# Optimization experiments

Hardware: AMD Instinct MI355X
Metric: run time of the kernel (lower is better)

Reference implementation:

```python
import jax, jax.numpy as jnp
import numpy as np

B, N, F_IN, F_OUT = 8, 4096, 256, 256


def setup_inputs() -> dict:
    key = jax.random.key(0)
    k1, k2, k3 = jax.random.split(key, 3)
    H = jax.random.normal(k1, (B, N, F_IN), dtype=jnp.float32)
    W = jax.random.normal(k2, (F_IN, F_OUT), dtype=jnp.float32) * (1.0 / np.sqrt(F_IN))
    A = jax.random.normal(k3, (N, N), dtype=jnp.float32) * (1.414 * np.sqrt(2.0 / (N + N)))
    return {"H": H, "W": W, "A": A}


def reference(H, W, A):
    # HW: [B, N, F_out]
    HW = jnp.einsum('bnf,fo->bno', H, W)
    # symmetrize + relu -> nonneg adjacency [N, N]
    A_norm = jax.nn.relu((A + A.T) * 0.5)
    # degree and inverse sqrt (inf -> 0 for isolated nodes)
    D = jnp.sum(A_norm, axis=1)
    D_safe = jnp.where(D > 0, D, 1.0)
    d_inv_sqrt = jnp.where(D > 0, D_safe ** -0.5, 0.0)
    # L_norm = I - D^{-1/2} A D^{-1/2}  (diagonal scaling, no dense diag matmul)
    DAD = d_inv_sqrt[:, None] * A_norm * d_inv_sqrt[None, :]
    L_norm = jnp.eye(N, dtype=H.dtype) - DAD
    # output = relu(L_norm @ HW): [B, N, F_out]
    out = jnp.einsum('nm,bmo->bno', L_norm, HW)
    return jax.nn.relu(out)
```

## Files before the change

kernel.cpp:

```cpp
#include <hip/hip_runtime.h>
#include <stdint.h>

#define N_NODES 4096
#define F_DIM   256
#define BATCH   8

typedef __attribute__((ext_vector_type(8))) __bf16 bf16x8;
typedef __attribute__((ext_vector_type(4))) float  f32x4;
typedef __attribute__((ext_vector_type(8))) unsigned short u16x8;

typedef const __attribute__((address_space(1))) void* gas1_t;
typedef __attribute__((address_space(3))) void*       las3_t;

__device__ __forceinline__ void stage16(const void* g, void* l) {
  __builtin_amdgcn_global_load_lds((gas1_t)g, (las3_t)l, 16, 0, 0);
}

__device__ __forceinline__ unsigned short f2bf(float f) {
  union { float f; uint32_t u; } v; v.f = f;
  uint32_t u = v.u;
  return (unsigned short)((u + 0x7FFFu + ((u >> 16) & 1u)) >> 16);
}
__device__ __forceinline__ float bf2f(unsigned short u) {
  union { uint32_t u; float f; } v; v.u = ((uint32_t)u) << 16;
  return v.f;
}

__global__ __launch_bounds__(256) void k_pre(const float* __restrict__ A,
                                             unsigned short* __restrict__ Sb,
                                             float* __restrict__ D,
                                             const float4* __restrict__ H4,
                                             ushort4* __restrict__ Hb4,
                                             const float* __restrict__ W,
                                             unsigned short* __restrict__ Wt) {
  int t = threadIdx.x;
  int bid = blockIdx.y * 64 + blockIdx.x;
  {
    int i = bid * 512 + t;
    float4 v = H4[i];
    ushort4 o; o.x = f2bf(v.x); o.y = f2bf(v.y); o.z = f2bf(v.z); o.w = f2bf(v.w);
    Hb4[i] = o;
    i += 256;
    v = H4[i];
    o.x = f2bf(v.x); o.y = f2bf(v.y); o.z = f2bf(v.z); o.w = f2bf(v.w);
    Hb4[i] = o;
  }
  if (bid < 256) Wt[t * 256 + bid] = f2bf(W[bid * 256 + t]);

  int bi = blockIdx.y, bj = blockIdx.x;
  if (bj < bi) return;
  __shared__ float L1[64][65];
  __shared__ float L2[64][65];
  __shared__ float Pr[4][64];
  __shared__ float Pc[4][64];
  int i0 = bi * 64, j0 = bj * 64;
  for (int it = 0; it < 16; ++it) {
    int idx = it * 256 + t;
    int r = idx >> 6, c = idx & 63;
    L1[r][c] = A[(size_t)(i0 + r) * N_NODES + (j0 + c)];
    L2[c][r] = A[(size_t)(j0 + r) * N_NODES + (i0 + c)];
  }
  __syncthreads();
  float colsum = 0.f;
  int cfix = t & 63, q = t >> 6;
  for (int it = 0; it < 16; ++it) {
    int r = it * 4 + q;
    float v = 0.5f * (L1[r][cfix] + L2[r][cfix]);
    v = v > 0.f ? v : 0.f;
    Sb[(size_t)(i0 + r) * N_NODES + (j0 + cfix)] = f2bf(v);
    colsum += v;
    L1[r][cfix] = v;
  }
  Pc[q][cfix] = colsum;
  __syncthreads();
  {
    int r = t & 63, seg = t >> 6;
    float s = 0.f;
    for (int c = seg * 16; c < seg * 16 + 16; ++c) s += L1[r][c];
    Pr[seg][r] = s;
  }
  __syncthreads();
  if (t < 64) {
    float d = Pr[0][t] + Pr[1][t] + Pr[2][t] + Pr[3][t];
    atomicAdd(&D[i0 + t], d);
  } else if (t < 128 && bi != bj) {
    int c = t - 64;
    float d = Pc[0][c] + Pc[1][c] + Pc[2][c] + Pc[3][c];
    atomicAdd(&D[j0 + c], d);
  }
  if (bi != bj) {
    for (int it = 0; it < 16; ++it) {
      int idx = it * 256 + t;
      int ro = idx >> 6, co = idx & 63;
      Sb[(size_t)(j0 + ro) * N_NODES + (i0 + co)] = f2bf(L1[co][ro]);
    }
  }
}

__global__ void k_dinv(const float* __restrict__ D, float* __restrict__ dinv) {
  int i = blockIdx.x * blockDim.x + threadIdx.x;
  if (i < N_NODES) {
    float d = D[i];
    dinv[i] = d > 0.f ? 1.0f / sqrtf(d) : 0.f;
  }
}

__global__ __launch_bounds__(256) void k_gemm1(const unsigned short* __restrict__ Hb,
                                               const unsigned short* __restrict__ Wt,
                                               const float* __restrict__ dinv,
                                               unsigned short* __restrict__ HWb,
                                               unsigned short* __restrict__ Gt) {
  __shared__ __align__(16) unsigned short As[128 * 32];
  __shared__ __align__(16) unsigned short Bs[128 * 32];
  __shared__ __align__(16) unsigned short T[128][136];
  int t = threadIdx.x;
  int lane = t & 63;
  int q = lane >> 4, r16 = lane & 15;
  int wave = t >> 6;
  int wm = wave >> 1, wn = wave & 1;
  int m0 = blockIdx.y * 128;
  int o0 = blockIdx.x * 128;
  const int K = 256;

  const unsigned short* Abase = Hb + (size_t)m0 * K;
  const unsigned short* Bbase = Wt + (size_t)o0 * K;

  f32x4 acc[4][4];
#pragma unroll
  for (int i = 0; i < 4; ++i)
#pragma unroll
    for (int j = 0; j < 4; ++j) acc[i][j] = f32x4{0.f, 0.f, 0.f, 0.f};

  int idx0 = t, idx1 = 256 + t;
  int wb0 = (t & ~63) * 8;
  int wb1 = (256 + (t & ~63)) * 8;

  for (int kt = 0; kt < K / 32; ++kt) {
    int kof = kt * 32;
    stage16(Abase + (size_t)(idx0 >> 2) * K + kof + ((idx0 & 3) << 3), &As[wb0]);
    stage16(Abase + (size_t)(idx1 >> 2) * K + kof + ((idx1 & 3) << 3), &As[wb1]);
    stage16(Bbase + (size_t)(idx0 >> 2) * K + kof + ((idx0 & 3) << 3), &Bs[wb0]);
    stage16(Bbase + (size_t)(idx1 >> 2) * K + kof + ((idx1 & 3) << 3), &Bs[wb1]);
    __syncthreads();
    bf16x8 a[4], b[4];
#pragma unroll
    for (int mi = 0; mi < 4; ++mi)
      a[mi] = *(const bf16x8*)&As[(wm * 64 + mi * 16 + r16) * 32 + q * 8];
#pragma unroll
    for (int ni = 0; ni < 4; ++ni)
      b[ni] = *(const bf16x8*)&Bs[(wn * 64 + ni * 16 + r16) * 32 + q * 8];
#pragma unroll
    for (int mi = 0; mi < 4; ++mi)
#pragma unroll
      for (int ni = 0; ni < 4; ++ni)
        acc[mi][ni] = __builtin_amdgcn_mfma_f32_16x16x32_bf16(a[mi], b[ni], acc[mi][ni], 0, 0, 0);
    __syncthreads();
  }

#pragma unroll
  for (int mi = 0; mi < 4; ++mi) {
    int row = wm * 64 + mi * 16 + q * 4;
#pragma unroll
    for (int ni = 0; ni < 4; ++ni) {
      int col = wn * 64 + ni * 16 + r16;
#pragma unroll
      for (int rr = 0; rr < 4; ++rr) {
        unsigned short h = f2bf(acc[mi][ni][rr]);
        HWb[(size_t)(m0 + row + rr) * F_DIM + (o0 + col)] = h;
        T[col][row + rr] = h;
      }
    }
  }
  __syncthreads();
  int b = m0 >> 12, n0 = m0 & 4095;
  for (int it = 0; it < 8; ++it) {
    int unit = it * 256 + t;
    int ro = unit >> 4;
    int cs = (unit & 15) * 8;
    u16x8 v = *(const u16x8*)&T[ro][cs];
    u16x8 w;
#pragma unroll
    for (int j = 0; j < 8; ++j)
      w[j] = f2bf(bf2f(v[j]) * dinv[n0 + cs + j]);
    *(u16x8*)&Gt[(size_t)(b * 256 + o0 + ro) * N_NODES + n0 + cs] = w;
  }
}

__global__ __launch_bounds__(256, 2) void k_gemm2(const unsigned short* __restrict__ Sb,
                                                  const unsigned short* __restrict__ Gt,
                                                  const unsigned short* __restrict__ HWb,
                                                  const float* __restrict__ dinv,
                                                  float* __restrict__ Out) {
  __shared__ __align__(16) unsigned short As[128 * 32];
  __shared__ __align__(16) unsigned short Bs[128 * 32];
  __shared__ float Red[64 * 130];
  const int K = N_NODES;
  int t = threadIdx.x;
  int lane = t & 63;
  int q = lane >> 4, r16 = lane & 15;
  int wave = t >> 6;
  int wm = wave >> 1;
  int kz = wave & 1;
  int m0 = blockIdx.y * 128;
  int n0 = blockIdx.x * 128;

  const unsigned short* Abase = Sb + (size_t)m0 * K;
  const unsigned short* Bbase = Gt + (size_t)n0 * K;

  f32x4 acc[4][8];
#pragma unroll
  for (int i = 0; i < 4; ++i)
#pragma unroll
    for (int j = 0; j < 8; ++j) acc[i][j] = f32x4{0.f, 0.f, 0.f, 0.f};

  int u0 = t, u1 = 256 + t;
  int r0 = u0 >> 2, q0 = ((u0 & 3) - (r0 >> 1)) & 3;
  int r1 = u1 >> 2, q1 = ((u1 & 3) - (r1 >> 1)) & 3;
  const unsigned short* pa0 = Abase + (size_t)r0 * K + q0 * 8;
  const unsigned short* pa1 = Abase + (size_t)r1 * K + q1 * 8;
  const unsigned short* pb0 = Bbase + (size_t)r0 * K + q0 * 8;
  const unsigned short* pb1 = Bbase + (size_t)r1 * K + q1 * 8;
  int wb0 = (t & ~63) * 8;
  int wb1 = (256 + (t & ~63)) * 8;

  int aoff[4], boff[8];
#pragma unroll
  for (int mi = 0; mi < 4; ++mi) {
    int row = wm * 64 + mi * 16 + r16;
    aoff[mi] = row * 32 + (((q + (row >> 1)) & 3) << 3);
  }
#pragma unroll
  for (int ni = 0; ni < 8; ++ni) {
    int row = ni * 16 + r16;
    boff[ni] = row * 32 + (((q + (row >> 1)) & 3) << 3);
  }

  for (int kt = 0; kt < K / 32; ++kt) {
    int kof = kt * 32;
    stage16(pa0 + kof, &As[wb0]);
    stage16(pa1 + kof, &As[wb1]);
    stage16(pb0 + kof, &Bs[wb0]);
    stage16(pb1 + kof, &Bs[wb1]);
    __syncthreads();
    if ((kt & 1) == kz) {
      bf16x8 a[4], b[8];
#pragma unroll
      for (int mi = 0; mi < 4; ++mi) a[mi] = *(const bf16x8*)&As[aoff[mi]];
#pragma unroll
      for (int ni = 0; ni < 8; ++ni) b[ni] = *(const bf16x8*)&Bs[boff[ni]];
#pragma unroll
      for (int mi = 0; mi < 4; ++mi)
#pragma unroll
        for (int ni = 0; ni < 8; ++ni)
          acc[mi][ni] = __builtin_amdgcn_mfma_f32_16x16x32_bf16(a[mi], b[ni], acc[mi][ni], 0, 0, 0);
    }
    __syncthreads();
  }

  for (int round = 0; round < 2; ++round) {
    if (wm == round && kz == 1) {
#pragma unroll
      for (int mi = 0; mi < 4; ++mi)
#pragma unroll
        for (int ni = 0; ni < 8; ++ni)
#pragma unroll
          for (int rr = 0; rr < 4; ++rr)
            Red[(mi * 16 + q * 4 + rr) * 130 + ni * 16 + r16] = acc[mi][ni][rr];
    }
    __syncthreads();
    if (wm == round && kz == 0) {
#pragma unroll
      for (int mi = 0; mi < 4; ++mi) {
        int row = m0 + wm * 64 + mi * 16 + q * 4;
        float di[4];
#pragma unroll
        for (int rr = 0; rr < 4; ++rr) di[rr] = dinv[row + rr];
#pragma unroll
        for (int ni = 0; ni < 8; ++ni) {
          int col = n0 + ni * 16 + r16;
          int b_ = col >> 8, o = col & 255;
#pragma unroll
          for (int rr = 0; rr < 4; ++rr) {
            float v = acc[mi][ni][rr] + Red[(mi * 16 + q * 4 + rr) * 130 + ni * 16 + r16];
            size_t oi = ((size_t)b_ * N_NODES + (row + rr)) * F_DIM + o;
            float u = bf2f(HWb[oi]) - di[rr] * v;
            Out[oi] = u > 0.f ? u : 0.f;
          }
        }
      }
    }
    __syncthreads();
  }
}

extern "C" void kernel_launch(void* const* d_in, const int* in_sizes, int n_in,
                              void* d_out, int out_size, void* d_ws, size_t ws_size,
                              hipStream_t stream) {
  (void)in_sizes; (void)n_in; (void)out_size; (void)ws_size;
  const float* H = (const float*)d_in[0];
  const float* W = (const float*)d_in[1];
  const float* A = (const float*)d_in[2];
  float* out = (float*)d_out;

  char* ws = (char*)d_ws;
  size_t off = 0;
  auto alloc = [&](size_t bytes) {
    char* p = ws + off;
    off += (bytes + 255) & ~(size_t)255;
    return p;
  };
  float*          Dd   = (float*)alloc((size_t)N_NODES * 4);
  float*          dinv = (float*)alloc((size_t)N_NODES * 4);
  unsigned short* Sb   = (unsigned short*)alloc((size_t)N_NODES * N_NODES * 2);
  unsigned short* HWb  = (unsigned short*)alloc((size_t)BATCH * N_NODES * F_DIM * 2);
  unsigned short* Gt   = (unsigned short*)alloc((size_t)BATCH * F_DIM * N_NODES * 2);
  unsigned short* Wt   = (unsigned short*)alloc((size_t)F_DIM * F_DIM * 2);
  unsigned short* Hb   = (unsigned short*)alloc((size_t)BATCH * N_NODES * F_DIM * 2);

  hipMemsetAsync(Dd, 0, N_NODES * 4, stream);
  k_pre<<<dim3(64, 64), 256, 0, stream>>>(A, Sb, Dd, (const float4*)H, (ushort4*)Hb, W, Wt);
  k_dinv<<<16, 256, 0, stream>>>(Dd, dinv);
  k_gemm1<<<dim3(2, 256), 256, 0, stream>>>(Hb, Wt, dinv, HWb, Gt);
  k_gemm2<<<dim3(16, 32), 256, 0, stream>>>(Sb, Gt, HWb, dinv, out);
}
```

Measured before the change: 260.0 us.

## Rewrite propagation GEMM to load fragments directly from global with register double-buffering

```diff
diff --git a/kernel.cpp b/kernel.cpp
--- a/kernel.cpp
+++ b/kernel.cpp
@@ -186,110 +186,104 @@
   }
 }
 
-__global__ __launch_bounds__(256, 2) void k_gemm2(const unsigned short* __restrict__ Sb,
-                                                  const unsigned short* __restrict__ Gt,
-                                                  const unsigned short* __restrict__ HWb,
-                                                  const float* __restrict__ dinv,
-                                                  float* __restrict__ Out) {
-  __shared__ __align__(16) unsigned short As[128 * 32];
-  __shared__ __align__(16) unsigned short Bs[128 * 32];
-  __shared__ float Red[64 * 130];
+__global__ __launch_bounds__(256) void k_gemm2(const unsigned short* __restrict__ Sb,
+                                               const unsigned short* __restrict__ Gt,
+                                               const unsigned short* __restrict__ HWb,
+                                               const float* __restrict__ dinv,
+                                               float* __restrict__ Out) {
   const int K = N_NODES;
-  int t = threadIdx.x;
-  int lane = t & 63;
+  int t = threadIdx.x, lane = t & 63, wv = t >> 6;
   int q = lane >> 4, r16 = lane & 15;
-  int wave = t >> 6;
-  int wm = wave >> 1;
-  int kz = wave & 1;
-  int m0 = blockIdx.y * 128;
-  int n0 = blockIdx.x * 128;
-
-  const unsigned short* Abase = Sb + (size_t)m0 * K;
-  const unsigned short* Bbase = Gt + (size_t)n0 * K;
-
-  f32x4 acc[4][8];
+
+  int bid = blockIdx.x;
+  int p = bid & 7, local = bid >> 3;
+  int mtg = p >> 1, ntg = p & 1;
+  int mt = mtg * 4 + (local & 3);
+  int nt = ntg * 16 + (local >> 2);
+  int m0 = mt * 256 + wv * 64;
+  int n0 = nt * 64;
+
+  const unsigned short* ap[4];
+  const unsigned short* bp[4];
+#pragma unroll
+  for (int mi = 0; mi < 4; ++mi)
+    ap[mi] = Sb + (size_t)(m0 + mi * 16 + r16) * K + q * 8;
+#pragma unroll
+  for (int ni = 0; ni < 4; ++ni)
+    bp[ni] = Gt + (size_t)(n0 + ni * 16 + r16) * K + q * 8;
+
+  f32x4 acc[4][4];
 #pragma unroll
   for (int i = 0; i < 4; ++i)
 #pragma unroll
-    for (int j = 0; j < 8; ++j) acc[i][j] = f32x4{0.f, 0.f, 0.f, 0.f};
-
-  int u0 = t, u1 = 256 + t;
-  int r0 = u0 >> 2, q0 = ((u0 & 3) - (r0 >> 1)) & 3;
-  int r1 = u1 >> 2, q1 = ((u1 & 3) - (r1 >> 1)) & 3;
-  const unsigned short* pa0 = Abase + (size_t)r0 * K + q0 * 8;
-  const unsigned short* pa1 = Abase + (size_t)r1 * K + q1 * 8;
-  const unsigned short* pb0 = Bbase + (size_t)r0 * K + q0 * 8;
-  const unsigned short* pb1 = Bbase + (size_t)r1 * K + q1 * 8;
-  int wb0 = (t & ~63) * 8;
-  int wb1 = (256 + (t & ~63)) * 8;
-
-  int aoff[4], boff[8];
+    for (int j = 0; j < 4; ++j) acc[i][j] = f32x4{0.f, 0.f, 0.f, 0.f};
+
+  bf16x8 a0[4], b0[4], a1[4], b1[4];
+#pragma unroll
+  for (int i = 0; i < 4; ++i) {
+    a0[i] = *(const bf16x8*)(ap[i]);
+    b0[i] = *(const bf16x8*)(bp[i]);
+  }
+
+  for (int kt = 0; kt < 126; kt += 2) {
+    int k1 = (kt + 1) * 32, k2 = (kt + 2) * 32;
+#pragma unroll
+    for (int i = 0; i < 4; ++i) {
+      a1[i] = *(const bf16x8*)(ap[i] + k1);
+      b1[i] = *(const bf16x8*)(bp[i] + k1);
+    }
+#pragma unroll
+    for (int mi = 0; mi < 4; ++mi)
+#pragma unroll
+      for (int ni = 0; ni < 4; ++ni)
+        acc[mi][ni] = __builtin_amdgcn_mfma_f32_16x16x32_bf16(a0[mi], b0[ni], acc[mi][ni], 0, 0, 0);
+#pragma unroll
+    for (int i = 0; i < 4; ++i) {
+      a0[i] = *(const bf16x8*)(ap[i] + k2);
+      b0[i] = *(const bf16x8*)(bp[i] + k2);
+    }
+#pragma unroll
+    for (int mi = 0; mi < 4; ++mi)
+#pragma unroll
+      for (int ni = 0; ni < 4; ++ni)
+        acc[mi][ni] = __builtin_amdgcn_mfma_f32_16x16x32_bf16(a1[mi], b1[ni], acc[mi][ni], 0, 0, 0);
+  }
+  {
+    int k1 = 127 * 32;
+#pragma unroll
+    for (int i = 0; i < 4; ++i) {
+      a1[i] = *(const bf16x8*)(ap[i] + k1);
+      b1[i] = *(const bf16x8*)(bp[i] + k1);
+    }
+#pragma unroll
+    for (int mi = 0; mi < 4; ++mi)
+#pragma unroll
+      for (int ni = 0; ni < 4; ++ni)
+        acc[mi][ni] = __builtin_amdgcn_mfma_f32_16x16x32_bf16(a0[mi], b0[ni], acc[mi][ni], 0, 0, 0);
+#pragma unroll
+    for (int mi = 0; mi < 4; ++mi)
+#pragma unroll
+      for (int ni = 0; ni < 4; ++ni)
+        acc[mi][ni] = __builtin_amdgcn_mfma_f32_16x16x32_bf16(a1[mi], b1[ni], acc[mi][ni], 0, 0, 0);
+  }
+
 #pragma unroll
   for (int mi = 0; mi < 4; ++mi) {
-    int row = wm * 64 + mi * 16 + r16;
-    aoff[mi] = row * 32 + (((q + (row >> 1)) & 3) << 3);
-  }
-#pragma unroll
-  for (int ni = 0; ni < 8; ++ni) {
-    int row = ni * 16 + r16;
-    boff[ni] = row * 32 + (((q + (row >> 1)) & 3) << 3);
-  }
-
-  for (int kt = 0; kt < K / 32; ++kt) {
-    int kof = kt * 32;
-    stage16(pa0 + kof, &As[wb0]);
-    stage16(pa1 + kof, &As[wb1]);
-    stage16(pb0 + kof, &Bs[wb0]);
-    stage16(pb1 + kof, &Bs[wb1]);
-    __syncthreads();
-    if ((kt & 1) == kz) {
-      bf16x8 a[4], b[8];
-#pragma unroll
-      for (int mi = 0; mi < 4; ++mi) a[mi] = *(const bf16x8*)&As[aoff[mi]];
-#pragma unroll
-      for (int ni = 0; ni < 8; ++ni) b[ni] = *(const bf16x8*)&Bs[boff[ni]];
-#pragma unroll
-      for (int mi = 0; mi < 4; ++mi)
-#pragma unroll
-        for (int ni = 0; ni < 8; ++ni)
-          acc[mi][ni] = __builtin_amdgcn_mfma_f32_16x16x32_bf16(a[mi], b[ni], acc[mi][ni], 0, 0, 0);
-    }
-    __syncthreads();
-  }
-
-  for (int round = 0; round < 2; ++round) {
-    if (wm == round && kz == 1) {
-#pragma unroll
-      for (int mi = 0; mi < 4; ++mi)
-#pragma unroll
-        for (int ni = 0; ni < 8; ++ni)
-#pragma unroll
-          for (int rr = 0; rr < 4; ++rr)
-            Red[(mi * 16 + q * 4 + rr) * 130 + ni * 16 + r16] = acc[mi][ni][rr];
-    }
-    __syncthreads();
-    if (wm == round && kz == 0) {
-#pragma unroll
-      for (int mi = 0; mi < 4; ++mi) {
-        int row = m0 + wm * 64 + mi * 16 + q * 4;
-        float di[4];
-#pragma unroll
-        for (int rr = 0; rr < 4; ++rr) di[rr] = dinv[row + rr];
-#pragma unroll
-        for (int ni = 0; ni < 8; ++ni) {
-          int col = n0 + ni * 16 + r16;
-          int b_ = col >> 8, o = col & 255;
-#pragma unroll
-          for (int rr = 0; rr < 4; ++rr) {
-            float v = acc[mi][ni][rr] + Red[(mi * 16 + q * 4 + rr) * 130 + ni * 16 + r16];
-            size_t oi = ((size_t)b_ * N_NODES + (row + rr)) * F_DIM + o;
-            float u = bf2f(HWb[oi]) - di[rr] * v;
-            Out[oi] = u > 0.f ? u : 0.f;
-          }
-        }
+    int row = m0 + mi * 16 + q * 4;
+    float di[4];
+#pragma unroll
+    for (int rr = 0; rr < 4; ++rr) di[rr] = dinv[row + rr];
+#pragma unroll
+    for (int ni = 0; ni < 4; ++ni) {
+      int col = n0 + ni * 16 + r16;
+      int b_ = col >> 8, o = col & 255;
+#pragma unroll
+      for (int rr = 0; rr < 4; ++rr) {
+        size_t oi = ((size_t)b_ * N_NODES + (row + rr)) * F_DIM + o;
+        float u = bf2f(HWb[oi]) - di[rr] * acc[mi][ni][rr];
+        Out[oi] = u > 0.f ? u : 0.f;
       }
     }
-    __syncthreads();
   }
 }
 
@@ -321,5 +315,5 @@
   k_pre<<<dim3(64, 64), 256, 0, stream>>>(A, Sb, Dd, (const float4*)H, (ushort4*)Hb, W, Wt);
   k_dinv<<<16, 256, 0, stream>>>(Dd, dinv);
   k_gemm1<<<dim3(2, 256), 256, 0, stream>>>(Hb, Wt, dinv, HWb, Gt);
-  k_gemm2<<<dim3(16, 32), 256, 0, stream>>>(Sb, Gt, HWb, dinv, out);
-}
+  k_gemm2<<<512, 256, 0, stream>>>(Sb, Gt, HWb, dinv, out);
+}
```

Measured after the change: 390.2 us. 50.1% more time.

## Retile gemm2 to 128x64 blocks with XCD-aware tile mapping, drop split-K

Applied to the files above, without the earlier changes.

```diff
diff --git a/kernel.cpp b/kernel.cpp
--- a/kernel.cpp
+++ b/kernel.cpp
@@ -186,110 +186,102 @@
   }
 }
 
-__global__ __launch_bounds__(256, 2) void k_gemm2(const unsigned short* __restrict__ Sb,
-                                                  const unsigned short* __restrict__ Gt,
-                                                  const unsigned short* __restrict__ HWb,
-                                                  const float* __restrict__ dinv,
-                                                  float* __restrict__ Out) {
+__global__ __launch_bounds__(128) void k_gemm2(const unsigned short* __restrict__ Sb,
+                                               const unsigned short* __restrict__ Gt,
+                                               const unsigned short* __restrict__ HWb,
+                                               const float* __restrict__ dinv,
+                                               float* __restrict__ Out) {
   __shared__ __align__(16) unsigned short As[128 * 32];
-  __shared__ __align__(16) unsigned short Bs[128 * 32];
-  __shared__ float Red[64 * 130];
+  __shared__ __align__(16) unsigned short Bs[64 * 32];
   const int K = N_NODES;
   int t = threadIdx.x;
   int lane = t & 63;
   int q = lane >> 4, r16 = lane & 15;
-  int wave = t >> 6;
-  int wm = wave >> 1;
-  int kz = wave & 1;
-  int m0 = blockIdx.y * 128;
-  int n0 = blockIdx.x * 128;
+  int wm = t >> 6;
+
+  int bid = blockIdx.x;
+  int xcd = bid & 7;
+  int local = bid >> 3;
+  int mt = xcd * 4 + (local >> 5);
+  int nt = local & 31;
+  int m0 = mt * 128;
+  int n0 = nt * 64;
 
   const unsigned short* Abase = Sb + (size_t)m0 * K;
   const unsigned short* Bbase = Gt + (size_t)n0 * K;
 
-  f32x4 acc[4][8];
+  f32x4 acc[4][4];
 #pragma unroll
   for (int i = 0; i < 4; ++i)
 #pragma unroll
-    for (int j = 0; j < 8; ++j) acc[i][j] = f32x4{0.f, 0.f, 0.f, 0.f};
-
-  int u0 = t, u1 = 256 + t;
-  int r0 = u0 >> 2, q0 = ((u0 & 3) - (r0 >> 1)) & 3;
-  int r1 = u1 >> 2, q1 = ((u1 & 3) - (r1 >> 1)) & 3;
-  const unsigned short* pa0 = Abase + (size_t)r0 * K + q0 * 8;
-  const unsigned short* pa1 = Abase + (size_t)r1 * K + q1 * 8;
-  const unsigned short* pb0 = Bbase + (size_t)r0 * K + q0 * 8;
-  const unsigned short* pb1 = Bbase + (size_t)r1 * K + q1 * 8;
-  int wb0 = (t & ~63) * 8;
-  int wb1 = (256 + (t & ~63)) * 8;
-
-  int aoff[4], boff[8];
+    for (int j = 0; j < 4; ++j) acc[i][j] = f32x4{0.f, 0.f, 0.f, 0.f};
+
+  size_t ga[4], gb[2];
+  int la[4], lb[2];
+#pragma unroll
+  for (int j = 0; j < 4; ++j) {
+    int u = j * 128 + t;
+    int r = u >> 2, qq = ((u & 3) - (r >> 1)) & 3;
+    ga[j] = (size_t)r * K + qq * 8;
+    la[j] = (j * 128 + (t & ~63)) * 8;
+  }
+#pragma unroll
+  for (int j = 0; j < 2; ++j) {
+    int u = j * 128 + t;
+    int r = u >> 2, qq = ((u & 3) - (r >> 1)) & 3;
+    gb[j] = (size_t)r * K + qq * 8;
+    lb[j] = (j * 128 + (t & ~63)) * 8;
+  }
+
+  int aoff[4], boff[4];
 #pragma unroll
   for (int mi = 0; mi < 4; ++mi) {
     int row = wm * 64 + mi * 16 + r16;
     aoff[mi] = row * 32 + (((q + (row >> 1)) & 3) << 3);
   }
 #pragma unroll
-  for (int ni = 0; ni < 8; ++ni) {
+  for (int ni = 0; ni < 4; ++ni) {
     int row = ni * 16 + r16;
     boff[ni] = row * 32 + (((q + (row >> 1)) & 3) << 3);
   }
 
   for (int kt = 0; kt < K / 32; ++kt) {
     int kof = kt * 32;
-    stage16(pa0 + kof, &As[wb0]);
-    stage16(pa1 + kof, &As[wb1]);
-    stage16(pb0 + kof, &Bs[wb0]);
-    stage16(pb1 + kof, &Bs[wb1]);
+#pragma unroll
+    for (int j = 0; j < 4; ++j) stage16(Abase + ga[j] + kof, &As[la[j]]);
+#pragma unroll
+    for (int j = 0; j < 2; ++j) stage16(Bbase + gb[j] + kof, &Bs[lb[j]]);
     __syncthreads();
-    if ((kt & 1) == kz) {
-      bf16x8 a[4], b[8];
-#pragma unroll
-      for (int mi = 0; mi < 4; ++mi) a[mi] = *(const bf16x8*)&As[aoff[mi]];
-#pragma unroll
-      for (int ni = 0; ni < 8; ++ni) b[ni] = *(const bf16x8*)&Bs[boff[ni]];
-#pragma unroll
-      for (int mi = 0; mi < 4; ++mi)
-#pragma unroll
-        for (int ni = 0; ni < 8; ++ni)
-          acc[mi][ni] = __builtin_amdgcn_mfma_f32_16x16x32_bf16(a[mi], b[ni], acc[mi][ni], 0, 0, 0);
-    }
+    bf16x8 a[4], b[4];
+#pragma unroll
+    for (int mi = 0; mi < 4; ++mi) a[mi] = *(const bf16x8*)&As[aoff[mi]];
+#pragma unroll
+    for (int ni = 0; ni < 4; ++ni) b[ni] = *(const bf16x8*)&Bs[boff[ni]];
+#pragma unroll
+    for (int mi = 0; mi < 4; ++mi)
+#pragma unroll
+      for (int ni = 0; ni < 4; ++ni)
+        acc[mi][ni] = __builtin_amdgcn_mfma_f32_16x16x32_bf16(a[mi], b[ni], acc[mi][ni], 0, 0, 0);
     __syncthreads();
   }
 
-  for (int round = 0; round < 2; ++round) {
-    if (wm == round && kz == 1) {
-#pragma unroll
-      for (int mi = 0; mi < 4; ++mi)
-#pragma unroll
-        for (int ni = 0; ni < 8; ++ni)
-#pragma unroll
-          for (int rr = 0; rr < 4; ++rr)
-            Red[(mi * 16 + q * 4 + rr) * 130 + ni * 16 + r16] = acc[mi][ni][rr];
-    }
-    __syncthreads();
-    if (wm == round && kz == 0) {
-#pragma unroll
-      for (int mi = 0; mi < 4; ++mi) {
-        int row = m0 + wm * 64 + mi * 16 + q * 4;
-        float di[4];
-#pragma unroll
-        for (int rr = 0; rr < 4; ++rr) di[rr] = dinv[row + rr];
-#pragma unroll
-        for (int ni = 0; ni < 8; ++ni) {
-          int col = n0 + ni * 16 + r16;
-          int b_ = col >> 8, o = col & 255;
-#pragma unroll
-          for (int rr = 0; rr < 4; ++rr) {
-            float v = acc[mi][ni][rr] + Red[(mi * 16 + q * 4 + rr) * 130 + ni * 16 + r16];
-            size_t oi = ((size_t)b_ * N_NODES + (row + rr)) * F_DIM + o;
-            float u = bf2f(HWb[oi]) - di[rr] * v;
-            Out[oi] = u > 0.f ? u : 0.f;
-          }
-        }
+#pragma unroll
+  for (int mi = 0; mi < 4; ++mi) {
+    int row = m0 + wm * 64 + mi * 16 + q * 4;
+    float di[4];
+#pragma unroll
+    for (int rr = 0; rr < 4; ++rr) di[rr] = dinv[row + rr];
+#pragma unroll
+    for (int ni = 0; ni < 4; ++ni) {
+      int col = n0 + ni * 16 + r16;
+      int b_ = col >> 8, o = col & 255;
+#pragma unroll
+      for (int rr = 0; rr < 4; ++rr) {
+        size_t oi = ((size_t)b_ * N_NODES + (row + rr)) * F_DIM + o;
+        float u = bf2f(HWb[oi]) - di[rr] * acc[mi][ni][rr];
+        Out[oi] = u > 0.f ? u : 0.f;
       }
     }
-    __syncthreads();
   }
 }
 
@@ -321,5 +313,5 @@
   k_pre<<<dim3(64, 64), 256, 0, stream>>>(A, Sb, Dd, (const float4*)H, (ushort4*)Hb, W, Wt);
   k_dinv<<<16, 256, 0, stream>>>(Dd, dinv);
   k_gemm1<<<dim3(2, 256), 256, 0, stream>>>(Hb, Wt, dinv, HWb, Gt);
-  k_gemm2<<<dim3(16, 32), 256, 0, stream>>>(Sb, Gt, HWb, dinv, out);
-}
+  k_gemm2<<<1024, 128, 0, stream>>>(Sb, Gt, HWb, dinv, out);
+}
```

Measured after the change: 260.7 us. Within noise of the previous version (+0.3%).
